# Optimization experiments

Measured on AMD Instinct MI355X. Metric: run time of the kernel, lower is better.

## Reference

```python
import jax, jax.numpy as jnp
import numpy as np

N = 50000      # total nodes
E = 600000     # edges
F_IN = 128     # dataset.num_features
G = 500        # graphs (100 nodes each)
K = 30         # sort-pool k
D1, D2, D3 = 64, 64, 1
DTOT = D1 + D2 + D3  # 129


def gcn_conv(x, W, b, src, dst, dinv, n):
    # PyG GCNConv: x' = D^-1/2 (A+I) D^-1/2 (x W) + b ; src/dst include self-loops
    h = x @ W
    norm = dinv[src] * dinv[dst]
    msg = h[src] * norm[:, None]
    return jax.ops.segment_sum(msg, dst, num_segments=n) + b


def setup_inputs():
    key = jax.random.key(0)
    ks = jax.random.split(key, 24)
    rn = lambda k, s, sc=0.1: jax.random.normal(k, s, dtype=jnp.float32) * sc
    return {
        "x": jax.random.normal(ks[0], (N, F_IN), dtype=jnp.float32),
        "edge_index": jax.random.randint(ks[1], (2, E), 0, N),
        "W1": rn(ks[2], (F_IN, D1)), "b1": rn(ks[3], (D1,)),
        "W2": rn(ks[4], (D1, D2)),  "b2": rn(ks[5], (D2,)),
        "W3": rn(ks[6], (D2, D3)),  "b3": rn(ks[7], (D3,)),
        "Ws1": rn(ks[8], (D1, 1)),  "bs1": rn(ks[9], (1,)),
        "Ws2": rn(ks[10], (D2, 1)), "bs2": rn(ks[11], (1,)),
        "Ws3": rn(ks[12], (D3, 1)), "bs3": rn(ks[13], (1,)),
        "Wc1": rn(ks[14], (16, 1, DTOT)), "bc1": rn(ks[15], (16,)),
        "Wc2": rn(ks[16], (32, 16, 5)),   "bc2": rn(ks[17], (32,)),
        "Wl1": rn(ks[18], (128, 352)),    "bl1": rn(ks[19], (128,)),
        "Wl2": rn(ks[20], (1, 128)),      "bl2": rn(ks[21], (1,)),
        "num_graphs": G,
    }


def reference(x, edge_index, W1, b1, W2, b2, W3, b3, Ws1, bs1, Ws2, bs2, Ws3, bs3,
              Wc1, bc1, Wc2, bc2, Wl1, bl1, Wl2, bl2, num_graphs):
    n = x.shape[0]
    loops = jnp.arange(n)
    src = jnp.concatenate([edge_index[0], loops])
    dst = jnp.concatenate([edge_index[1], loops])
    deg = jnp.zeros((n,), jnp.float32).at[dst].add(1.0)
    dinv = jnp.where(deg > 0, deg ** -0.5, 0.0)

    h = jax.nn.relu(gcn_conv(x, W1, b1, src, dst, dinv, n))
    x1 = gcn_conv(h, Ws1, bs1, src, dst, dinv, n) * h
    h = jax.nn.relu(gcn_conv(h, W2, b2, src, dst, dinv, n))
    x2 = gcn_conv(h, Ws2, bs2, src, dst, dinv, n) * h
    h = jax.nn.relu(gcn_conv(h, W3, b3, src, dst, dinv, n))
    x3 = gcn_conv(h, Ws3, bs3, src, dst, dinv, n) * h
    feats = jnp.concatenate([x1, x2, x3], axis=1)  # [N, 129]

    # global_sort_pool: equal-size graphs (batch = id // npg), sort desc by last channel, keep top-K
    npg = n // num_graphs
    fg = feats.reshape(num_graphs, npg, DTOT)
    order = jnp.argsort(-fg[:, :, -1], axis=1)[:, :K]                 # [G, K]
    pooled = jnp.take_along_axis(fg, order[:, :, None], axis=1)       # [G, K, 129]

    # Conv1d(1->16, kernel=129, stride=129) == per-position dense over the 129-dim blocks
    c1 = jax.nn.relu(jnp.einsum('gkd,cd->gck', pooled, Wc1[:, 0, :]) + bc1[None, :, None])  # [G,16,30]
    mp = c1.reshape(num_graphs, 16, K // 2, 2).max(axis=-1)           # MaxPool1d(2,2) -> [G,16,15]
    c2 = jax.lax.conv_general_dilated(mp, Wc2, window_strides=(1,), padding='VALID',
                                      dimension_numbers=('NCH', 'OIH', 'NCH')) + bc2[None, :, None]
    c2 = jax.nn.relu(c2)                                              # [G,32,11]
    flat = c2.reshape(num_graphs, -1)                                 # [G,352]
    hdd = jax.nn.relu(flat @ Wl1.T + bl1)
    out = hdd @ Wl2.T + bl2
    return out[:, 0]
```

## Files before the change

kernel.cpp:

```cpp
#include <hip/hip_runtime.h>
#include <hip/hip_bf16.h>

#define NN 50000
#define EE 600000
#define FIN 128
#define GG 500
#define NPG 100
#define KK 30
#define SCHUNK 1024

__global__ void psg_deg(const int* __restrict__ dst, int* __restrict__ deg, int e) {
    int i = blockIdx.x * blockDim.x + threadIdx.x;
    if (i < e) atomicAdd(&deg[dst[i]], 1);
}

__global__ __launch_bounds__(SCHUNK) void psg_scan1(const int* __restrict__ deg,
                                                    int* __restrict__ rowptr,
                                                    int* __restrict__ csums,
                                                    float* __restrict__ dinv, int n) {
    __shared__ int sm[SCHUNK];
    int t = threadIdx.x;
    int base = blockIdx.x * SCHUNK;
    int v = (base + t < n) ? deg[base + t] : 0;
    sm[t] = v;
    __syncthreads();
    for (int off = 1; off < SCHUNK; off <<= 1) {
        int u = (t >= off) ? sm[t - off] : 0;
        __syncthreads();
        sm[t] += u;
        __syncthreads();
    }
    if (base + t < n) {
        rowptr[base + t] = sm[t] - v;
        dinv[base + t] = 1.0f / sqrtf((float)(v + 1));
    }
    if (t == SCHUNK - 1) csums[blockIdx.x] = sm[t];
}

__global__ void psg_scan2(int* __restrict__ csums, int nb) {
    int t = threadIdx.x;
    int v = (t < nb) ? csums[t] : 0;
    int x = v;
#pragma unroll
    for (int off = 1; off < 64; off <<= 1) {
        int u = __shfl_up(x, off, 64);
        if (t >= off) x += u;
    }
    if (t < nb) csums[t] = x - v;
}

__global__ __launch_bounds__(SCHUNK) void psg_scan3(int* __restrict__ rowptr,
                                                    int* __restrict__ rowfill,
                                                    const int* __restrict__ csums,
                                                    int n, int e) {
    int i = blockIdx.x * SCHUNK + threadIdx.x;
    if (i < n) {
        int v = rowptr[i] + csums[blockIdx.x];
        rowptr[i] = v;
        rowfill[i] = v;
    }
    if (i == 0) rowptr[n] = e;
}

__global__ void psg_build(const int* __restrict__ src, const int* __restrict__ dst,
                          int* __restrict__ rowfill, int* __restrict__ csr_src, int e) {
    int i = blockIdx.x * blockDim.x + threadIdx.x;
    if (i < e) {
        int pos = atomicAdd(&rowfill[dst[i]], 1);
        csr_src[pos] = src[i];
    }
}

template <int KD>
__global__ __launch_bounds__(256) void psg_gemm(const float* __restrict__ X,
                                                const float* __restrict__ W,
                                                const float* __restrict__ dinv,
                                                float* __restrict__ hs, int n) {
    __shared__ __align__(16) float Xl[16][KD];
    __shared__ __align__(16) float WtF[(KD / 4) * 64 * 4];
    int t = threadIdx.x;
    int r0 = blockIdx.x * 16;
    for (int i = t; i < KD * 64; i += 256) {
        int k = i >> 6, j = i & 63;
        WtF[(((k >> 2) * 64 + j) << 2) + (k & 3)] = W[i];
    }
    for (int i4 = t; i4 < 16 * (KD / 4); i4 += 256) {
        int r = i4 / (KD / 4), u = i4 % (KD / 4);
        int row = r0 + r;
        float4 v = make_float4(0.f, 0.f, 0.f, 0.f);
        if (row < n) v = ((const float4*)(X + (size_t)row * KD))[u];
        ((float4*)&Xl[r][0])[u] = v;
    }
    __syncthreads();
    int j = t & 63, q = t >> 6;
    const float4* Wt4 = (const float4*)WtF;
    float a0 = 0.f, a1 = 0.f, a2 = 0.f, a3 = 0.f;
#pragma unroll 4
    for (int u = 0; u < KD / 4; ++u) {
        float4 wv = Wt4[u * 64 + j];
        float4 x0 = *(const float4*)&Xl[q * 4 + 0][u * 4];
        float4 x1 = *(const float4*)&Xl[q * 4 + 1][u * 4];
        float4 x2 = *(const float4*)&Xl[q * 4 + 2][u * 4];
        float4 x3 = *(const float4*)&Xl[q * 4 + 3][u * 4];
        a0 += x0.x * wv.x + x0.y * wv.y + x0.z * wv.z + x0.w * wv.w;
        a1 += x1.x * wv.x + x1.y * wv.y + x1.z * wv.z + x1.w * wv.w;
        a2 += x2.x * wv.x + x2.y * wv.y + x2.z * wv.z + x2.w * wv.w;
        a3 += x3.x * wv.x + x3.y * wv.y + x3.z * wv.z + x3.w * wv.w;
    }
    float av[4] = {a0, a1, a2, a3};
#pragma unroll
    for (int rr = 0; rr < 4; rr++) {
        int row = r0 + q * 4 + rr;
        if (row < n) hs[(size_t)row * 64 + j] = av[rr] * dinv[row];
    }
}

template <int NDOT>
__global__ __launch_bounds__(256) void psg_gfin(const float* __restrict__ hs,
                                                const int* __restrict__ rowptr,
                                                const int* __restrict__ csr_src,
                                                const float* __restrict__ dinv,
                                                const float* __restrict__ b,
                                                float* __restrict__ h,
                                                const float* __restrict__ wv0,
                                                float* __restrict__ s0_src,
                                                const float* __restrict__ wv1,
                                                float* __restrict__ s1_src, int n) {
    int w = (int)((blockIdx.x * 256 + threadIdx.x) >> 6);
    int j = threadIdx.x & 63;
    if (w >= n) return;
    int p0 = rowptr[w], p1 = rowptr[w + 1];
    float a0 = hs[(size_t)w * 64 + j];
    float a1 = 0.f, a2 = 0.f, a3 = 0.f, a4 = 0.f, a5 = 0.f, a6 = 0.f, a7 = 0.f;
    int p = p0;
    for (; p + 8 <= p1; p += 8) {
        int s0 = csr_src[p],     s1 = csr_src[p + 1], s2 = csr_src[p + 2], s3 = csr_src[p + 3];
        int s4 = csr_src[p + 4], s5 = csr_src[p + 5], s6 = csr_src[p + 6], s7 = csr_src[p + 7];
        a0 += hs[(size_t)s0 * 64 + j];
        a1 += hs[(size_t)s1 * 64 + j];
        a2 += hs[(size_t)s2 * 64 + j];
        a3 += hs[(size_t)s3 * 64 + j];
        a4 += hs[(size_t)s4 * 64 + j];
        a5 += hs[(size_t)s5 * 64 + j];
        a6 += hs[(size_t)s6 * 64 + j];
        a7 += hs[(size_t)s7 * 64 + j];
    }
    if (p + 4 <= p1) {
        int s0 = csr_src[p], s1 = csr_src[p + 1], s2 = csr_src[p + 2], s3 = csr_src[p + 3];
        a4 += hs[(size_t)s0 * 64 + j];
        a5 += hs[(size_t)s1 * 64 + j];
        a6 += hs[(size_t)s2 * 64 + j];
        a7 += hs[(size_t)s3 * 64 + j];
        p += 4;
    }
    for (; p < p1; ++p) a1 += hs[(size_t)csr_src[p] * 64 + j];
    float a = ((a0 + a1) + (a2 + a3)) + ((a4 + a5) + (a6 + a7));
    float di = dinv[w];
    float v = fmaxf(a * di + b[j], 0.f);
    h[(size_t)w * 64 + j] = v;
    float t0 = v * wv0[j];
#pragma unroll
    for (int o = 32; o; o >>= 1) t0 += __shfl_xor(t0, o, 64);
    if (j == 0) s0_src[w] = t0 * di;
    if (NDOT == 2) {
        float t1 = v * wv1[j];
#pragma unroll
        for (int o = 32; o; o >>= 1) t1 += __shfl_xor(t1, o, 64);
        if (j == 0) s1_src[w] = t1 * di;
    }
}

__global__ void psg_h3g(const float* __restrict__ sc_src,
                        const int* __restrict__ rowptr, const int* __restrict__ csr_src,
                        const float* __restrict__ dinv, const float* __restrict__ b3,
                        const float* __restrict__ Ws3,
                        float* __restrict__ h3, float* __restrict__ u_src, int n) {
    int i = blockIdx.x * blockDim.x + threadIdx.x;
    if (i < n) {
        float a = sc_src[i];
        int p1 = rowptr[i + 1];
        for (int p = rowptr[i]; p < p1; ++p) a += sc_src[csr_src[p]];
        float di = dinv[i];
        float v = fmaxf(a * di + b3[0], 0.f);
        h3[i] = v;
        u_src[i] = v * Ws3[0] * di;
    }
}

__device__ __forceinline__ int psg_f2ord(float f) {
    int s = __float_as_int(f);
    return s < 0 ? (s ^ 0x7fffffff) : s;
}

__global__ __launch_bounds__(128) void psg_sortpool(const float* __restrict__ u_src,
                                                    const int* __restrict__ rowptr,
                                                    const int* __restrict__ csr_src,
                                                    const float* __restrict__ dinv,
                                                    const float* __restrict__ bs1,
                                                    const float* __restrict__ bs2,
                                                    const float* __restrict__ bs3,
                                                    const float* __restrict__ sA_src,
                                                    const float* __restrict__ sB_src,
                                                    const float* __restrict__ h1,
                                                    const float* __restrict__ h2,
                                                    const float* __restrict__ h3,
                                                    float* __restrict__ pooled) {
    int g = blockIdx.x, t = threadIdx.x;
    __shared__ float key[NPG];
    __shared__ int ord[NPG];
    __shared__ int sel[KK];
    __shared__ float sa[KK], sb[KK];
    if (t < NPG) {
        int node = g * NPG + t;
        float a = u_src[node];
        int pe = rowptr[node + 1];
        for (int p = rowptr[node]; p < pe; ++p) a += u_src[csr_src[p]];
        float v = (a * dinv[node] + bs3[0]) * h3[node];
        key[t] = v;
        ord[t] = psg_f2ord(v);
    }
    __syncthreads();
    if (t < NPG) {
        int v = ord[t];
        int r = 0;
        for (int m = 0; m < NPG; m++) {
            int u = ord[m];
            r += (u > v) || (u == v && m < t);
        }
        if (r < KK) sel[r] = t;
    }
    __syncthreads();
    {
        int r = t & 31;
        if (t < 64 && r < KK) {
            int node = g * NPG + sel[r];
            const float* ssrc = (t < 32) ? sA_src : sB_src;
            float a = ssrc[node];
            int pe = rowptr[node + 1];
            for (int p = rowptr[node]; p < pe; ++p) a += ssrc[csr_src[p]];
            float scl = a * dinv[node] + ((t < 32) ? bs1[0] : bs2[0]);
            if (t < 32) sa[r] = scl; else sb[r] = scl;
        }
    }
    __syncthreads();
    for (int idx = t; idx < KK * 129; idx += 128) {
        int r = idx / 129, c = idx - r * 129;
        int node = g * NPG + sel[r];
        float v;
        if (c < 64) v = sa[r] * h1[(size_t)node * 64 + c];
        else if (c < 128) v = sb[r] * h2[(size_t)node * 64 + (c - 64)];
        else v = key[sel[r]];
        pooled[((size_t)g * KK + r) * 129 + c] = v;
    }
}

__global__ __launch_bounds__(128) void psg_cnn(const float* __restrict__ pooled,
                                               const float* __restrict__ Wc1, const float* __restrict__ bc1,
                                               const float* __restrict__ Wc2, const float* __restrict__ bc2,
                                               const float* __restrict__ Wl1, const float* __restrict__ bl1,
                                               const float* __restrict__ Wl2, const float* __restrict__ bl2,
                                               float* __restrict__ out) {
    int g = blockIdx.x, t = threadIdx.x;
    __shared__ float pl[KK * 129];
    __shared__ float wc1[16 * 129];
    __shared__ float wc2[32 * 16 * 5];
    __shared__ float c1[16 * KK];
    __shared__ float mp[16 * 15];
    __shared__ float c2s[352];
    __shared__ float hdds[128];
    __shared__ float red[2];
    for (int i = t; i < KK * 129; i += 128) pl[i] = pooled[(size_t)g * KK * 129 + i];
    for (int i = t; i < 16 * 129; i += 128) wc1[i] = Wc1[i];
    for (int i = t; i < 32 * 16 * 5; i += 128) wc2[i] = Wc2[i];
    __syncthreads();
    for (int idx = t; idx < 16 * KK; idx += 128) {
        int c = idx / KK, k = idx % KK;
        float a = bc1[c];
        for (int d = 0; d < 129; d++) a += pl[k * 129 + d] * wc1[c * 129 + d];
        c1[c * KK + k] = fmaxf(a, 0.f);
    }
    __syncthreads();
    for (int idx = t; idx < 16 * 15; idx += 128) {
        int c = idx / 15, k = idx % 15;
        mp[idx] = fmaxf(c1[c * KK + 2 * k], c1[c * KK + 2 * k + 1]);
    }
    __syncthreads();
    for (int idx = t; idx < 352; idx += 128) {
        int o = idx / 11, k = idx % 11;
        float a = bc2[o];
        for (int i2 = 0; i2 < 16; i2++) {
#pragma unroll
            for (int k2 = 0; k2 < 5; k2++) a += mp[i2 * 15 + k + k2] * wc2[(o * 16 + i2) * 5 + k2];
        }
        c2s[o * 11 + k] = fmaxf(a, 0.f);
    }
    __syncthreads();
    {
        float a = bl1[t];
        const float* wr = Wl1 + (size_t)t * 352;
        for (int f = 0; f < 352; f++) a += c2s[f] * wr[f];
        hdds[t] = fmaxf(a, 0.f);
    }
    __syncthreads();
    float p = hdds[t] * Wl2[t];
#pragma unroll
    for (int o = 32; o; o >>= 1) p += __shfl_xor(p, o, 64);
    if ((t & 63) == 0) red[t >> 6] = p;
    __syncthreads();
    if (t == 0) out[g] = red[0] + red[1] + bl2[0];
}

extern "C" void kernel_launch(void* const* d_in, const int* in_sizes, int n_in,
                              void* d_out, int out_size, void* d_ws, size_t ws_size,
                              hipStream_t stream) {
    const float* x   = (const float*)d_in[0];
    const int*   ei  = (const int*)d_in[1];
    const float* W1  = (const float*)d_in[2];
    const float* b1  = (const float*)d_in[3];
    const float* W2  = (const float*)d_in[4];
    const float* b2  = (const float*)d_in[5];
    const float* W3  = (const float*)d_in[6];
    const float* b3  = (const float*)d_in[7];
    const float* Ws1 = (const float*)d_in[8];
    const float* bs1 = (const float*)d_in[9];
    const float* Ws2 = (const float*)d_in[10];
    const float* bs2 = (const float*)d_in[11];
    const float* Ws3 = (const float*)d_in[12];
    const float* bs3 = (const float*)d_in[13];
    const float* Wc1 = (const float*)d_in[14];
    const float* bc1 = (const float*)d_in[15];
    const float* Wc2 = (const float*)d_in[16];
    const float* bc2 = (const float*)d_in[17];
    const float* Wl1 = (const float*)d_in[18];
    const float* bl1 = (const float*)d_in[19];
    const float* Wl2 = (const float*)d_in[20];
    const float* bl2 = (const float*)d_in[21];
    float* out = (float*)d_out;

    const int n = in_sizes[0] / FIN;
    const int e = in_sizes[1] / 2;
    const int* src = ei;
    const int* dst = ei + e;
    const int nchunk = (n + SCHUNK - 1) / SCHUNK;

    char* w = (char*)d_ws;
    float* dinv    = (float*)w; w += (size_t)n * 4;
    float* sA_src  = (float*)w; w += (size_t)n * 4;
    float* sB_src  = (float*)w; w += (size_t)n * 4;
    float* sC_src  = (float*)w; w += (size_t)n * 4;
    float* h3      = (float*)w; w += (size_t)n * 4;
    float* u_src   = (float*)w; w += (size_t)n * 4;
    int*   deg     = (int*)w;   w += (size_t)n * 4;
    int*   rowptr  = (int*)w;   w += (size_t)(n + 1) * 4;
    int*   rowfill = (int*)w;   w += (size_t)n * 4;
    int*   csums   = (int*)w;   w += 64 * 4;
    int*   csr_src = (int*)w;   w += (size_t)e * 4;
    float* hs      = (float*)w; w += (size_t)n * 64 * 4;
    float* h1      = (float*)w; w += (size_t)n * 64 * 4;
    float* h2      = (float*)w; w += (size_t)n * 64 * 4;
    float* pooled  = (float*)w; w += (size_t)GG * KK * 129 * 4;

    const int nb_e  = (e + 255) / 256;
    const int nb_n  = (n + 255) / 256;
    const int nb_g  = (n + 15) / 16;
    const int nb_nw = (n * 64 + 255) / 256;

    hipMemsetAsync(deg, 0, (size_t)n * 4, stream);
    psg_deg<<<nb_e, 256, 0, stream>>>(dst, deg, e);
    psg_scan1<<<nchunk, SCHUNK, 0, stream>>>(deg, rowptr, csums, dinv, n);
    psg_scan2<<<1, 64, 0, stream>>>(csums, nchunk);
    psg_scan3<<<nchunk, SCHUNK, 0, stream>>>(rowptr, rowfill, csums, n, e);
    psg_build<<<nb_e, 256, 0, stream>>>(src, dst, rowfill, csr_src, e);

    psg_gemm<128><<<nb_g, 256, 0, stream>>>(x, W1, dinv, hs, n);
    psg_gfin<1><<<nb_nw, 256, 0, stream>>>(hs, rowptr, csr_src, dinv, b1, h1,
                                           Ws1, sA_src, nullptr, nullptr, n);

    psg_gemm<64><<<nb_g, 256, 0, stream>>>(h1, W2, dinv, hs, n);
    psg_gfin<2><<<nb_nw, 256, 0, stream>>>(hs, rowptr, csr_src, dinv, b2, h2,
                                           Ws2, sB_src, W3, sC_src, n);

    psg_h3g<<<nb_n, 256, 0, stream>>>(sC_src, rowptr, csr_src, dinv, b3, Ws3, h3, u_src, n);

    psg_sortpool<<<GG, 128, 0, stream>>>(u_src, rowptr, csr_src, dinv, bs1, bs2, bs3,
                                         sA_src, sB_src, h1, h2, h3, pooled);
    psg_cnn<<<GG, 128, 0, stream>>>(pooled, Wc1, bc1, Wc2, bc2, Wl1, bl1, Wl2, bl2, out);

    (void)n_in; (void)out_size; (void)ws_size;
}
```

Baseline: 355.0 us.

## Fuse layer-2 GEMM into gather, merge sortpool with CNN, drop scan2

```diff
diff --git a/kernel.cpp b/kernel.cpp
--- a/kernel.cpp
+++ b/kernel.cpp
@@ -37,25 +37,22 @@
     if (t == SCHUNK - 1) csums[blockIdx.x] = sm[t];
 }
 
-__global__ void psg_scan2(int* __restrict__ csums, int nb) {
-    int t = threadIdx.x;
-    int v = (t < nb) ? csums[t] : 0;
-    int x = v;
-#pragma unroll
-    for (int off = 1; off < 64; off <<= 1) {
-        int u = __shfl_up(x, off, 64);
-        if (t >= off) x += u;
-    }
-    if (t < nb) csums[t] = x - v;
-}
-
 __global__ __launch_bounds__(SCHUNK) void psg_scan3(int* __restrict__ rowptr,
                                                     int* __restrict__ rowfill,
                                                     const int* __restrict__ csums,
                                                     int n, int e) {
-    int i = blockIdx.x * SCHUNK + threadIdx.x;
+    __shared__ int soff;
+    int t = threadIdx.x;
+    if (t < 64) {
+        int c = (t < (int)blockIdx.x) ? csums[t] : 0;
+#pragma unroll
+        for (int o = 1; o < 64; o <<= 1) c += __shfl_xor(c, o, 64);
+        if (t == 0) soff = c;
+    }
+    __syncthreads();
+    int i = blockIdx.x * SCHUNK + t;
     if (i < n) {
-        int v = rowptr[i] + csums[blockIdx.x];
+        int v = rowptr[i] + soff;
         rowptr[i] = v;
         rowfill[i] = v;
     }
@@ -115,7 +112,7 @@
     }
 }
 
-template <int NDOT>
+template <int NDOT, bool FUSE>
 __global__ __launch_bounds__(256) void psg_gfin(const float* __restrict__ hs,
                                                 const int* __restrict__ rowptr,
                                                 const int* __restrict__ csr_src,
@@ -125,48 +122,70 @@
                                                 const float* __restrict__ wv0,
                                                 float* __restrict__ s0_src,
                                                 const float* __restrict__ wv1,
-                                                float* __restrict__ s1_src, int n) {
-    int w = (int)((blockIdx.x * 256 + threadIdx.x) >> 6);
-    int j = threadIdx.x & 63;
-    if (w >= n) return;
-    int p0 = rowptr[w], p1 = rowptr[w + 1];
-    float a0 = hs[(size_t)w * 64 + j];
-    float a1 = 0.f, a2 = 0.f, a3 = 0.f, a4 = 0.f, a5 = 0.f, a6 = 0.f, a7 = 0.f;
-    int p = p0;
-    for (; p + 8 <= p1; p += 8) {
-        int s0 = csr_src[p],     s1 = csr_src[p + 1], s2 = csr_src[p + 2], s3 = csr_src[p + 3];
-        int s4 = csr_src[p + 4], s5 = csr_src[p + 5], s6 = csr_src[p + 6], s7 = csr_src[p + 7];
-        a0 += hs[(size_t)s0 * 64 + j];
-        a1 += hs[(size_t)s1 * 64 + j];
-        a2 += hs[(size_t)s2 * 64 + j];
-        a3 += hs[(size_t)s3 * 64 + j];
-        a4 += hs[(size_t)s4 * 64 + j];
-        a5 += hs[(size_t)s5 * 64 + j];
-        a6 += hs[(size_t)s6 * 64 + j];
-        a7 += hs[(size_t)s7 * 64 + j];
-    }
-    if (p + 4 <= p1) {
-        int s0 = csr_src[p], s1 = csr_src[p + 1], s2 = csr_src[p + 2], s3 = csr_src[p + 3];
-        a4 += hs[(size_t)s0 * 64 + j];
-        a5 += hs[(size_t)s1 * 64 + j];
-        a6 += hs[(size_t)s2 * 64 + j];
-        a7 += hs[(size_t)s3 * 64 + j];
-        p += 4;
-    }
-    for (; p < p1; ++p) a1 += hs[(size_t)csr_src[p] * 64 + j];
-    float a = ((a0 + a1) + (a2 + a3)) + ((a4 + a5) + (a6 + a7));
-    float di = dinv[w];
-    float v = fmaxf(a * di + b[j], 0.f);
-    h[(size_t)w * 64 + j] = v;
-    float t0 = v * wv0[j];
-#pragma unroll
-    for (int o = 32; o; o >>= 1) t0 += __shfl_xor(t0, o, 64);
-    if (j == 0) s0_src[w] = t0 * di;
-    if (NDOT == 2) {
-        float t1 = v * wv1[j];
-#pragma unroll
-        for (int o = 32; o; o >>= 1) t1 += __shfl_xor(t1, o, 64);
-        if (j == 0) s1_src[w] = t1 * di;
+                                                float* __restrict__ s1_src,
+                                                const float* __restrict__ Wn,
+                                                float* __restrict__ hs_next, int n) {
+    __shared__ float Wnl[64 * 64];
+    int t = threadIdx.x;
+    if (FUSE) {
+        for (int i = t; i < 64 * 64; i += 256) Wnl[i] = Wn[i];
+    }
+    int w = (int)((blockIdx.x * 256 + t) >> 6);
+    int j = t & 63;
+    bool valid = (w < n);
+    float v = 0.f, di = 0.f;
+    if (valid) {
+        int p0 = rowptr[w], p1 = rowptr[w + 1];
+        float a0 = hs[(size_t)w * 64 + j];
+        float a1 = 0.f, a2 = 0.f, a3 = 0.f, a4 = 0.f, a5 = 0.f, a6 = 0.f, a7 = 0.f;
+        int p = p0;
+        for (; p + 8 <= p1; p += 8) {
+            int s0 = csr_src[p],     s1 = csr_src[p + 1], s2 = csr_src[p + 2], s3 = csr_src[p + 3];
+            int s4 = csr_src[p + 4], s5 = csr_src[p + 5], s6 = csr_src[p + 6], s7 = csr_src[p + 7];
+            a0 += hs[(size_t)s0 * 64 + j];
+            a1 += hs[(size_t)s1 * 64 + j];
+            a2 += hs[(size_t)s2 * 64 + j];
+            a3 += hs[(size_t)s3 * 64 + j];
+            a4 += hs[(size_t)s4 * 64 + j];
+            a5 += hs[(size_t)s5 * 64 + j];
+            a6 += hs[(size_t)s6 * 64 + j];
+            a7 += hs[(size_t)s7 * 64 + j];
+        }
+        if (p + 4 <= p1) {
+            int s0 = csr_src[p], s1 = csr_src[p + 1], s2 = csr_src[p + 2], s3 = csr_src[p + 3];
+            a4 += hs[(size_t)s0 * 64 + j];
+            a5 += hs[(size_t)s1 * 64 + j];
+            a6 += hs[(size_t)s2 * 64 + j];
+            a7 += hs[(size_t)s3 * 64 + j];
+            p += 4;
+        }
+        for (; p < p1; ++p) a1 += hs[(size_t)csr_src[p] * 64 + j];
+        float a = ((a0 + a1) + (a2 + a3)) + ((a4 + a5) + (a6 + a7));
+        di = dinv[w];
+        v = fmaxf(a * di + b[j], 0.f);
+        h[(size_t)w * 64 + j] = v;
+        float t0 = v * wv0[j];
+#pragma unroll
+        for (int o = 32; o; o >>= 1) t0 += __shfl_xor(t0, o, 64);
+        if (j == 0) s0_src[w] = t0 * di;
+        if (NDOT == 2) {
+            float t1 = v * wv1[j];
+#pragma unroll
+            for (int o = 32; o; o >>= 1) t1 += __shfl_xor(t1, o, 64);
+            if (j == 0) s1_src[w] = t1 * di;
+        }
+    }
+    if (FUSE) {
+        __syncthreads();
+        if (valid) {
+            float a2 = 0.f;
+#pragma unroll 8
+            for (int jj = 0; jj < 64; ++jj) {
+                float vj = __shfl(v, jj, 64);
+                a2 += vj * Wnl[jj * 64 + j];
+            }
+            hs_next[(size_t)w * 64 + j] = a2 * di;
+        }
     }
 }
 
@@ -192,24 +211,38 @@
     return s < 0 ? (s ^ 0x7fffffff) : s;
 }
 
-__global__ __launch_bounds__(128) void psg_sortpool(const float* __restrict__ u_src,
-                                                    const int* __restrict__ rowptr,
-                                                    const int* __restrict__ csr_src,
-                                                    const float* __restrict__ dinv,
-                                                    const float* __restrict__ bs1,
-                                                    const float* __restrict__ bs2,
-                                                    const float* __restrict__ bs3,
-                                                    const float* __restrict__ sA_src,
-                                                    const float* __restrict__ sB_src,
-                                                    const float* __restrict__ h1,
-                                                    const float* __restrict__ h2,
-                                                    const float* __restrict__ h3,
-                                                    float* __restrict__ pooled) {
+__global__ __launch_bounds__(128) void psg_spcnn(const float* __restrict__ u_src,
+                                                 const int* __restrict__ rowptr,
+                                                 const int* __restrict__ csr_src,
+                                                 const float* __restrict__ dinv,
+                                                 const float* __restrict__ bs1,
+                                                 const float* __restrict__ bs2,
+                                                 const float* __restrict__ bs3,
+                                                 const float* __restrict__ sA_src,
+                                                 const float* __restrict__ sB_src,
+                                                 const float* __restrict__ h1,
+                                                 const float* __restrict__ h2,
+                                                 const float* __restrict__ h3,
+                                                 const float* __restrict__ Wc1, const float* __restrict__ bc1,
+                                                 const float* __restrict__ Wc2, const float* __restrict__ bc2,
+                                                 const float* __restrict__ Wl1, const float* __restrict__ bl1,
+                                                 const float* __restrict__ Wl2, const float* __restrict__ bl2,
+                                                 float* __restrict__ out) {
     int g = blockIdx.x, t = threadIdx.x;
+    __shared__ float pl[KK * 129];
+    __shared__ float wc1l[16 * 129];
+    __shared__ float wc2l[32 * 16 * 5];
     __shared__ float key[NPG];
     __shared__ int ord[NPG];
     __shared__ int sel[KK];
     __shared__ float sa[KK], sb[KK];
+    __shared__ float c1[16 * KK];
+    __shared__ float mp[16 * 15];
+    __shared__ float c2s[352];
+    __shared__ float hdds[128];
+    __shared__ float red[2];
+    for (int i = t; i < 16 * 129; i += 128) wc1l[i] = Wc1[i];
+    for (int i = t; i < 32 * 16 * 5; i += 128) wc2l[i] = Wc2[i];
     if (t < NPG) {
         int node = g * NPG + t;
         float a = u_src[node];
@@ -250,33 +283,13 @@
         if (c < 64) v = sa[r] * h1[(size_t)node * 64 + c];
         else if (c < 128) v = sb[r] * h2[(size_t)node * 64 + (c - 64)];
         else v = key[sel[r]];
-        pooled[((size_t)g * KK + r) * 129 + c] = v;
-    }
-}
-
-__global__ __launch_bounds__(128) void psg_cnn(const float* __restrict__ pooled,
-                                               const float* __restrict__ Wc1, const float* __restrict__ bc1,
-                                               const float* __restrict__ Wc2, const float* __restrict__ bc2,
-                                               const float* __restrict__ Wl1, const float* __restrict__ bl1,
-                                               const float* __restrict__ Wl2, const float* __restrict__ bl2,
-                                               float* __restrict__ out) {
-    int g = blockIdx.x, t = threadIdx.x;
-    __shared__ float pl[KK * 129];
-    __shared__ float wc1[16 * 129];
-    __shared__ float wc2[32 * 16 * 5];
-    __shared__ float c1[16 * KK];
-    __shared__ float mp[16 * 15];
-    __shared__ float c2s[352];
-    __shared__ float hdds[128];
-    __shared__ float red[2];
-    for (int i = t; i < KK * 129; i += 128) pl[i] = pooled[(size_t)g * KK * 129 + i];
-    for (int i = t; i < 16 * 129; i += 128) wc1[i] = Wc1[i];
-    for (int i = t; i < 32 * 16 * 5; i += 128) wc2[i] = Wc2[i];
+        pl[idx] = v;
+    }
     __syncthreads();
     for (int idx = t; idx < 16 * KK; idx += 128) {
         int c = idx / KK, k = idx % KK;
         float a = bc1[c];
-        for (int d = 0; d < 129; d++) a += pl[k * 129 + d] * wc1[c * 129 + d];
+        for (int d = 0; d < 129; d++) a += pl[k * 129 + d] * wc1l[c * 129 + d];
         c1[c * KK + k] = fmaxf(a, 0.f);
     }
     __syncthreads();
@@ -290,7 +303,7 @@
         float a = bc2[o];
         for (int i2 = 0; i2 < 16; i2++) {
 #pragma unroll
-            for (int k2 = 0; k2 < 5; k2++) a += mp[i2 * 15 + k + k2] * wc2[(o * 16 + i2) * 5 + k2];
+            for (int k2 = 0; k2 < 5; k2++) a += mp[i2 * 15 + k + k2] * wc2l[(o * 16 + i2) * 5 + k2];
         }
         c2s[o * 11 + k] = fmaxf(a, 0.f);
     }
@@ -355,10 +368,10 @@
     int*   rowfill = (int*)w;   w += (size_t)n * 4;
     int*   csums   = (int*)w;   w += 64 * 4;
     int*   csr_src = (int*)w;   w += (size_t)e * 4;
-    float* hs      = (float*)w; w += (size_t)n * 64 * 4;
+    float* hs1     = (float*)w; w += (size_t)n * 64 * 4;
+    float* hs2     = (float*)w; w += (size_t)n * 64 * 4;
     float* h1      = (float*)w; w += (size_t)n * 64 * 4;
     float* h2      = (float*)w; w += (size_t)n * 64 * 4;
-    float* pooled  = (float*)w; w += (size_t)GG * KK * 129 * 4;
 
     const int nb_e  = (e + 255) / 256;
     const int nb_n  = (n + 255) / 256;
@@ -368,23 +381,23 @@
     hipMemsetAsync(deg, 0, (size_t)n * 4, stream);
     psg_deg<<<nb_e, 256, 0, stream>>>(dst, deg, e);
     psg_scan1<<<nchunk, SCHUNK, 0, stream>>>(deg, rowptr, csums, dinv, n);
-    psg_scan2<<<1, 64, 0, stream>>>(csums, nchunk);
     psg_scan3<<<nchunk, SCHUNK, 0, stream>>>(rowptr, rowfill, csums, n, e);
     psg_build<<<nb_e, 256, 0, stream>>>(src, dst, rowfill, csr_src, e);
 
-    psg_gemm<128><<<nb_g, 256, 0, stream>>>(x, W1, dinv, hs, n);
-    psg_gfin<1><<<nb_nw, 256, 0, stream>>>(hs, rowptr, csr_src, dinv, b1, h1,
-                                           Ws1, sA_src, nullptr, nullptr, n);
-
-    psg_gemm<64><<<nb_g, 256, 0, stream>>>(h1, W2, dinv, hs, n);
-    psg_gfin<2><<<nb_nw, 256, 0, stream>>>(hs, rowptr, csr_src, dinv, b2, h2,
-                                           Ws2, sB_src, W3, sC_src, n);
+    psg_gemm<128><<<nb_g, 256, 0, stream>>>(x, W1, dinv, hs1, n);
+    psg_gfin<1, true><<<nb_nw, 256, 0, stream>>>(hs1, rowptr, csr_src, dinv, b1, h1,
+                                                 Ws1, sA_src, nullptr, nullptr,
+                                                 W2, hs2, n);
+
+    psg_gfin<2, false><<<nb_nw, 256, 0, stream>>>(hs2, rowptr, csr_src, dinv, b2, h2,
+                                                  Ws2, sB_src, W3, sC_src,
+                                                  nullptr, nullptr, n);
 
     psg_h3g<<<nb_n, 256, 0, stream>>>(sC_src, rowptr, csr_src, dinv, b3, Ws3, h3, u_src, n);
 
-    psg_sortpool<<<GG, 128, 0, stream>>>(u_src, rowptr, csr_src, dinv, bs1, bs2, bs3,
-                                         sA_src, sB_src, h1, h2, h3, pooled);
-    psg_cnn<<<GG, 128, 0, stream>>>(pooled, Wc1, bc1, Wc2, bc2, Wl1, bl1, Wl2, bl2, out);
+    psg_spcnn<<<GG, 128, 0, stream>>>(u_src, rowptr, csr_src, dinv, bs1, bs2, bs3,
+                                      sA_src, sB_src, h1, h2, h3,
+                                      Wc1, bc1, Wc2, bc2, Wl1, bl1, Wl2, bl2, out);
 
     (void)n_in; (void)out_size; (void)ws_size;
 }
```

After: 369.3 us. 4.0% more time.
